# Kernel optimization log

Hardware: AMD Instinct MI355X
Metric: run time of the kernel (lower is better)

The kernel has to match this reference:

```python
import jax, jax.numpy as jnp
import numpy as np

N = 50000      # nodes
E = 800000     # edges (avg degree 16)
DIN = 128      # input_dim
DG = 128       # gnn_dim
DCLS = 128     # cls_dim
DOUT = 10      # output_dim
LMDA = 1.0     # rw_lmda
P_DROP = 0.5


def setup_inputs() -> dict:
    key = jax.random.key(0)
    ks = jax.random.split(key, 12)
    x = jax.random.normal(ks[0], (N, DIN), jnp.float32)
    edge_index = jax.random.randint(ks[1], (2, E), 0, N, dtype=jnp.int64)
    edge_weight = jax.random.uniform(ks[2], (E,), jnp.float32)
    def glorot(k, shape):
        lim = np.sqrt(6.0 / (shape[0] + shape[1])).astype(np.float32)
        return jax.random.uniform(k, shape, jnp.float32, -lim, lim)
    return dict(
        x=x, edge_index=edge_index, edge_weight=edge_weight,
        W_lin_in=glorot(ks[3], (DIN, DG)), b_lin_in=jnp.zeros((DG,), jnp.float32),
        W_agg_in=glorot(ks[4], (DG + DIN, DG)), b_agg_in=jnp.zeros((DG,), jnp.float32),
        W_lin_h=glorot(ks[5], (DG, DG)), b_lin_h=jnp.zeros((DG,), jnp.float32),
        W_agg_h=glorot(ks[6], (2 * DG, DG)), b_agg_h=jnp.zeros((DG,), jnp.float32),
        W_mlp1=glorot(ks[7], (DG, DCLS)), b_mlp1=jnp.zeros((DCLS,), jnp.float32),
        W_mlp2=glorot(ks[8], (DCLS, DOUT)), b_mlp2=jnp.zeros((DOUT,), jnp.float32),
    )


def _gs_layer(x, row, col, ew, inv_cnt, W_lin, b_lin, W_agg, b_agg):
    # GS_reweight: message = (1-lmda)*lin(x_j) + lmda*ew*lin(x_j), mean-aggregated
    # at row (flow='target_to_source': gather from col, scatter to row).
    h = x @ W_lin + b_lin                      # [N, DG] (lin before gather == lin(x_j))
    hj = h[col]                                # [E, DG] gather
    m = (1.0 - LMDA) * hj + LMDA * (ew[:, None] * hj)
    agg = jax.ops.segment_sum(m, row, num_segments=N) * inv_cnt[:, None]  # mean
    out = jnp.concatenate([agg, x], axis=-1) @ W_agg + b_agg              # update()
    return jax.nn.relu(out)


def _dropout(x, k):
    mask = jax.random.bernoulli(k, 1.0 - P_DROP, x.shape)
    return jnp.where(mask, x / (1.0 - P_DROP), 0.0)


def reference(x, edge_index, edge_weight,
              W_lin_in, b_lin_in, W_agg_in, b_agg_in,
              W_lin_h, b_lin_h, W_agg_h, b_agg_h,
              W_mlp1, b_mlp1, W_mlp2, b_mlp2):
    row, col = edge_index[0], edge_index[1]
    cnt = jax.ops.segment_sum(jnp.ones((E,), x.dtype), row, num_segments=N)
    inv_cnt = 1.0 / jnp.maximum(cnt, 1.0)     # scatter_mean: empty rows -> 0
    dk = jax.random.split(jax.random.key(42), 3)
    h = _gs_layer(x, row, col, edge_weight, inv_cnt, W_lin_in, b_lin_in, W_agg_in, b_agg_in)
    h = _dropout(jax.nn.relu(h), dk[0])       # relu is idempotent after update's relu
    for i in range(2):                        # layers 2,3 share prop_hidden weights
        h = _gs_layer(h, row, col, edge_weight, inv_cnt, W_lin_h, b_lin_h, W_agg_h, b_agg_h)
        h = _dropout(jax.nn.relu(h), dk[i + 1])
    y = jax.nn.relu(h @ W_mlp1 + b_mlp1) @ W_mlp2 + b_mlp2  # cls_layers=2, bn=False
    return (h, y)
```

## Files before the change

kernel.cpp:

```cpp
#include <hip/hip_runtime.h>
#include <cstdint>
#include <cstddef>


#define N_NODES 50000
#define N_EDGES 800000
#define DGN 128
#define DOUT 10
#define NELEM (N_NODES * DGN)
#define NMASKW (NELEM / 64)
#define NBINS 391
#define TILE 4096
#define NTILES ((N_EDGES + TILE - 1) / TILE)

#define XB_BLK 6250
#define MK_BLK 25000
#define HI_BLK NTILES
#define WC_BLK 128
#define TR_BLK 192
#define R0 XB_BLK
#define R1 (R0 + MK_BLK)
#define R2 (R1 + HI_BLK)
#define R3 (R2 + WC_BLK)
#define R4 (R3 + TR_BLK)
#define MEGA_BLOCKS (R4 + 1)

typedef __attribute__((ext_vector_type(8))) short bf16x8;
typedef __attribute__((ext_vector_type(4))) float f32x4;

__host__ __device__ static inline unsigned short f2bf(float f) {
  union { float f; unsigned u; } c; c.f = f;
  unsigned u = c.u;
  return (unsigned short)((u + 0x7fffu + ((u >> 16) & 1u)) >> 16);
}
__device__ static inline float bflo(unsigned u) { return __uint_as_float(u << 16); }
__device__ static inline float bfhi(unsigned u) { return __uint_as_float(u & 0xffff0000u); }

__host__ __device__ static inline void tf2x32(unsigned k0, unsigned k1,
                                              unsigned c0, unsigned c1,
                                              unsigned& o0, unsigned& o1) {
  unsigned ks2 = k0 ^ k1 ^ 0x1BD11BDAu;
  unsigned x0 = c0 + k0;
  unsigned x1 = c1 + k1;
#define TFR(r) { x0 += x1; x1 = (x1 << (r)) | (x1 >> (32 - (r))); x1 ^= x0; }
  TFR(13) TFR(15) TFR(26) TFR(6)
  x0 += k1;  x1 += ks2 + 1u;
  TFR(17) TFR(29) TFR(16) TFR(24)
  x0 += ks2; x1 += k0 + 2u;
  TFR(13) TFR(15) TFR(26) TFR(6)
  x0 += k0;  x1 += k1 + 3u;
  TFR(17) TFR(29) TFR(16) TFR(24)
  x0 += k1;  x1 += ks2 + 4u;
  TFR(13) TFR(15) TFR(26) TFR(6)
  x0 += ks2; x1 += k0 + 5u;
#undef TFR
  o0 = x0; o1 = x1;
}

__global__ __launch_bounds__(256) void mega_kernel(
    const float* __restrict__ x, unsigned short* __restrict__ xb,
    unsigned long long* __restrict__ m0, unsigned long long* __restrict__ m1,
    unsigned long long* __restrict__ m2,
    unsigned k00, unsigned k01, unsigned k10, unsigned k11,
    unsigned k20, unsigned k21,
    const int* __restrict__ ei, int* __restrict__ chist,
    const float* __restrict__ Wli, const float* __restrict__ Wai,
    const float* __restrict__ Wlh, const float* __restrict__ Wah,
    const float* __restrict__ Wm1,
    const float* __restrict__ bli, const float* __restrict__ blh,
    unsigned short* __restrict__ Tai, unsigned short* __restrict__ Tah,
    unsigned short* __restrict__ Tm1,
    float* __restrict__ bvi, float* __restrict__ bvh) {
  __shared__ int h[NBINS];
  const int b = blockIdx.x;
  const int tid = threadIdx.x;

  if (b < R0) {
    int g = b * 256 + tid;
    float4 v = ((const float4*)x)[g];
    ushort4 o;
    o.x = f2bf(v.x); o.y = f2bf(v.y); o.z = f2bf(v.z); o.w = f2bf(v.w);
    ((ushort4*)xb)[g] = o;
  } else if (b < R1) {
    int i = (b - R0) * 256 + tid;
    unsigned o0, o1;
    tf2x32(k00, k01, 0u, (unsigned)i, o0, o1);
    unsigned long long b0 = __ballot(((o0 ^ o1) >> 31) == 0u);
    tf2x32(k10, k11, 0u, (unsigned)i, o0, o1);
    unsigned long long b1 = __ballot(((o0 ^ o1) >> 31) == 0u);
    tf2x32(k20, k21, 0u, (unsigned)i, o0, o1);
    unsigned long long b2 = __ballot(((o0 ^ o1) >> 31) == 0u);
    if ((tid & 63) == 0) {
      int w = i >> 6;
      m0[w] = b0; m1[w] = b1; m2[w] = b2;
    }
  } else if (b < R2) {
    for (int i = tid; i < NBINS; i += 256) h[i] = 0;
    __syncthreads();
    const int e0 = (b - R1) * TILE;
#pragma unroll 4
    for (int j = 0; j < TILE; j += 256) {
      int e = e0 + j + tid;
      if (e < N_EDGES) {
        int r = ei[e];
        r = (r < 0) ? 0 : (r >= N_NODES ? N_NODES - 1 : r);
        atomicAdd(&h[r >> 7], 1);
      }
    }
    __syncthreads();
    for (int i = tid; i < NBINS; i += 256)
      if (h[i]) atomicAdd(&chist[i], h[i]);
  } else if (b < R3) {
    int idx = (b - R2) * 256 + tid;
    int n = idx & 127;
    int k = (idx >> 7) & 127;
    int m = idx >> 14;
    const float* Wl = m ? Wlh : Wli;
    const float* Wa = m ? Wah : Wai;
    unsigned short* T = m ? Tah : Tai;
    float acc = 0.0f;
#pragma unroll 8
    for (int j = 0; j < 128; ++j)
      acc += Wl[k * 128 + j] * Wa[j * 128 + n];
    T[n * 256 + k] = f2bf(acc);
  } else if (b < R4) {
    int j = (b - R3) * 256 + tid;
    if (j < 16384) {
      int kk = j & 127, n = j >> 7;
      Tai[n * 256 + 128 + kk] = f2bf(Wai[(size_t)(128 + kk) * 128 + n]);
    } else if (j < 32768) {
      int q = j - 16384;
      int kk = q & 127, n = q >> 7;
      Tah[n * 256 + 128 + kk] = f2bf(Wah[(size_t)(128 + kk) * 128 + n]);
    } else {
      int q = j - 32768;
      int k = q & 127, n = q >> 7;
      Tm1[n * 128 + k] = f2bf(Wm1[(size_t)k * 128 + n]);
    }
  } else {
    int n = tid & 127;
    const float* bl = (tid < 128) ? bli : blh;
    const float* Wa = (tid < 128) ? Wai : Wah;
    float acc = 0.0f;
    for (int j = 0; j < 128; ++j) acc += bl[j] * Wa[j * 128 + n];
    if (tid < 128) bvi[n] = acc; else bvh[n] = acc;
  }
}

__global__ __launch_bounds__(512) void prefix_kernel(const int* __restrict__ chist,
                                                     int* __restrict__ cbase,
                                                     int* __restrict__ ccursor,
                                                     int* __restrict__ rowptr) {
  __shared__ int s[512];
  const int t = threadIdx.x;
  int v = (t < NBINS) ? chist[t] : 0;
  s[t] = v;
  __syncthreads();
  for (int off = 1; off < 512; off <<= 1) {
    int tv = (t >= off) ? s[t - off] : 0;
    __syncthreads();
    s[t] += tv;
    __syncthreads();
  }
  if (t <= NBINS) {
    int ex = (t == 0) ? 0 : s[t - 1];
    cbase[t] = ex;
    if (t < NBINS) ccursor[t] = ex;
  }
  if (t == 0) rowptr[N_NODES] = N_EDGES;
}

__global__ __launch_bounds__(256) void scatter_kernel(const int* __restrict__ ei,
                                                      const float* __restrict__ ew,
                                                      int* __restrict__ ccursor,
                                                      uint2* __restrict__ pk) {
  __shared__ uint2 st[TILE];
  __shared__ unsigned short sbin[TILE];
  __shared__ int h[NBINS];
  __shared__ int base[NBINS];
  __shared__ int gbase[NBINS];
  __shared__ int cur[NBINS];
  __shared__ int sc[512];
  const int tid = threadIdx.x;
  const int e0 = blockIdx.x * TILE;
  const int nt = (N_EDGES - e0 < TILE) ? (N_EDGES - e0) : TILE;

  for (int i = tid; i < NBINS; i += 256) { h[i] = 0; cur[i] = 0; }
  __syncthreads();
  for (int j = tid; j < nt; j += 256) {
    int r = ei[e0 + j];
    r = (r < 0) ? 0 : (r >= N_NODES ? N_NODES - 1 : r);
    atomicAdd(&h[r >> 7], 1);
  }
  __syncthreads();
  sc[tid] = (tid < NBINS) ? h[tid] : 0;
  sc[tid + 256] = (tid + 256 < NBINS) ? h[tid + 256] : 0;
  __syncthreads();
  for (int off = 1; off < 512; off <<= 1) {
    int a0 = (tid >= off) ? sc[tid - off] : 0;
    int a1 = (tid + 256 >= off) ? sc[tid + 256 - off] : 0;
    __syncthreads();
    sc[tid] += a0; sc[tid + 256] += a1;
    __syncthreads();
  }
  if (tid < NBINS) {
    base[tid] = sc[tid] - h[tid];
    if (h[tid]) gbase[tid] = atomicAdd(&ccursor[tid], h[tid]);
  }
  if (tid + 256 < NBINS) {
    base[tid + 256] = sc[tid + 256] - h[tid + 256];
    if (h[tid + 256]) gbase[tid + 256] = atomicAdd(&ccursor[tid + 256], h[tid + 256]);
  }
  __syncthreads();
  for (int j = tid; j < nt; j += 256) {
    int r = ei[e0 + j];
    r = (r < 0) ? 0 : (r >= N_NODES ? N_NODES - 1 : r);
    int c = ei[N_EDGES + e0 + j];
    c = (c < 0) ? 0 : (c >= N_NODES ? N_NODES - 1 : c);
    int bb = r >> 7;
    int slot = base[bb] + atomicAdd(&cur[bb], 1);
    uint2 p;
    p.x = ((unsigned)r << 16) | (unsigned)c;
    p.y = __float_as_uint(ew[e0 + j]);
    st[slot] = p;
    sbin[slot] = (unsigned short)bb;
  }
  __syncthreads();
  for (int j = tid; j < nt; j += 256) {
    int bb = sbin[j];
    pk[gbase[bb] + (j - base[bb])] = st[j];
  }
}

__global__ __launch_bounds__(256) void place_kernel(const int* __restrict__ cbase,
                                                    const uint2* __restrict__ pk,
                                                    uint2* __restrict__ csr,
                                                    int* __restrict__ rowptr,
                                                    float* __restrict__ invc) {
  __shared__ int lcnt[128];
  __shared__ int lpre[128];
  __shared__ int lcur[128];
  __shared__ int sc[128];
  const int b = blockIdx.x;
  const int tid = threadIdx.x;
  const int cb = cbase[b];
  const int n = cbase[b + 1] - cb;
  const int r0 = b << 7;
  const int nr = (N_NODES - r0 < 128) ? (N_NODES - r0) : 128;

  if (tid < 128) { lcnt[tid] = 0; lcur[tid] = 0; }
  __syncthreads();
  for (int i = tid; i < n; i += 256) {
    int r7 = (int)(pk[cb + i].x >> 16) - r0;
    atomicAdd(&lcnt[r7], 1);
  }
  __syncthreads();
  if (tid < 128) sc[tid] = lcnt[tid];
  __syncthreads();
  for (int off = 1; off < 128; off <<= 1) {
    int tv = (tid >= off && tid < 128) ? sc[tid - off] : 0;
    __syncthreads();
    if (tid < 128) sc[tid] += tv;
    __syncthreads();
  }
  if (tid < 128) lpre[tid] = sc[tid] - lcnt[tid];
  __syncthreads();
  if (tid < nr) {
    rowptr[r0 + tid] = cb + lpre[tid];
    int c = lcnt[tid];
    invc[r0 + tid] = 1.0f / (float)(c > 1 ? c : 1);
  }
  for (int i = tid; i < n; i += 256) {
    uint2 p = pk[cb + i];
    int r7 = (int)(p.x >> 16) - r0;
    int slot = cb + lpre[r7] + atomicAdd(&lcur[r7], 1);
    uint2 o;
    o.x = p.x & 0xFFFFu;
    o.y = p.y;
    csr[slot] = o;
  }
}

__global__ __launch_bounds__(256) void agg_kernel(const unsigned short* __restrict__ hlin,
                                                  const int* __restrict__ rowptr,
                                                  const uint2* __restrict__ csr,
                                                  const float* __restrict__ invc,
                                                  unsigned short* __restrict__ agg,
                                                  float* __restrict__ swout) {
  const int r = blockIdx.x * 4 + (threadIdx.x >> 6);
  const int lane = threadIdx.x & 63;
  const int es = lane >> 4;
  const int cg = lane & 15;
  const int start = rowptr[r];
  const int num = rowptr[r + 1] - start;
  const uint4* __restrict__ H = (const uint4*)hlin;

  float a[8] = {0.f, 0.f, 0.f, 0.f, 0.f, 0.f, 0.f, 0.f};
  float ws = 0.f;
  for (int e = 0; e < num; e += 16) {
#pragma unroll
    for (int j = 0; j < 4; ++j) {
      int idx = e + j * 4 + es;
      bool ok = idx < num;
      int idxc = ok ? idx : (num - 1);
      uint2 q = csr[start + idxc];
      float w = ok ? __uint_as_float(q.y) : 0.0f;
      uint4 p = H[(size_t)q.x * 16 + cg];
      ws += w;
      a[0] += w * bflo(p.x); a[1] += w * bfhi(p.x);
      a[2] += w * bflo(p.y); a[3] += w * bfhi(p.y);
      a[4] += w * bflo(p.z); a[5] += w * bfhi(p.z);
      a[6] += w * bflo(p.w); a[7] += w * bfhi(p.w);
    }
  }
#pragma unroll
  for (int k = 0; k < 8; ++k) {
    a[k] += __shfl_xor(a[k], 32);
    a[k] += __shfl_xor(a[k], 16);
  }
  ws += __shfl_xor(ws, 32);
  ws += __shfl_xor(ws, 16);
  const float s = invc[r];
  if (es == 0) {
    uint4 o;
    o.x = (unsigned)f2bf(a[0] * s) | ((unsigned)f2bf(a[1] * s) << 16);
    o.y = (unsigned)f2bf(a[2] * s) | ((unsigned)f2bf(a[3] * s) << 16);
    o.z = (unsigned)f2bf(a[4] * s) | ((unsigned)f2bf(a[5] * s) << 16);
    o.w = (unsigned)f2bf(a[6] * s) | ((unsigned)f2bf(a[7] * s) << 16);
    ((uint4*)agg)[(size_t)r * 16 + cg] = o;
  }
  if (swout && lane == 0) swout[r] = ws * s;
}

template <int KTOT, bool RELU, bool MASK, bool SWB, bool WF32, bool WBF>
__global__ __launch_bounds__(256) void mfma_gemm(
    const unsigned short* __restrict__ A0, const unsigned short* __restrict__ A1,
    const unsigned short* __restrict__ Wt, const float* __restrict__ bias,
    const float* __restrict__ bias2, const float* __restrict__ sw,
    const unsigned long long* __restrict__ maskw,
    float* __restrict__ outf, unsigned short* __restrict__ outb) {
  constexpr int LDK = 72;
  __shared__ unsigned short Als[64 * LDK];
  __shared__ unsigned short Bls[64 * LDK];
  const int tid = threadIdx.x;
  const int mt = blockIdx.x >> 1;
  const int nt = blockIdx.x & 1;
  const int m0 = mt * 64;
  const int lane = tid & 63;
  const int wid = tid >> 6;
  const int wm = (wid >> 1) * 32;
  const int wn = (wid & 1) * 32;
  const int lrow = tid >> 2;
  const int lk = (tid & 3) * 16;

  int arow = m0 + lrow;
  if (arow >= N_NODES) arow = N_NODES - 1;

  f32x4 acc[2][2];
#pragma unroll
  for (int i = 0; i < 2; ++i)
#pragma unroll
    for (int j = 0; j < 2; ++j)
#pragma unroll
      for (int r = 0; r < 4; ++r) acc[i][j][r] = 0.0f;

  for (int kb = 0; kb < KTOT; kb += 64) {
    const unsigned short* Asrc = (kb < 128) ? A0 : A1;
    const unsigned short* ap = Asrc + (size_t)arow * 128 + (kb & 127) + lk;
    const unsigned short* bp = Wt + (size_t)(nt * 64 + lrow) * KTOT + kb + lk;
    unsigned short* al = &Als[lrow * LDK + lk];
    unsigned short* bl = &Bls[lrow * LDK + lk];
    *(uint4*)(al + 0) = *(const uint4*)(ap + 0);
    *(uint4*)(al + 8) = *(const uint4*)(ap + 8);
    *(uint4*)(bl + 0) = *(const uint4*)(bp + 0);
    *(uint4*)(bl + 8) = *(const uint4*)(bp + 8);
    __syncthreads();
#pragma unroll
    for (int ks = 0; ks < 64; ks += 32) {
      bf16x8 af[2], bfr[2];
#pragma unroll
      for (int t = 0; t < 2; ++t) {
        af[t]  = *(const bf16x8*)&Als[(wm + t * 16 + (lane & 15)) * LDK + ks + (lane >> 4) * 8];
        bfr[t] = *(const bf16x8*)&Bls[(wn + t * 16 + (lane & 15)) * LDK + ks + (lane >> 4) * 8];
      }
#pragma unroll
      for (int i = 0; i < 2; ++i)
#pragma unroll
        for (int j = 0; j < 2; ++j)
          acc[i][j] = __builtin_amdgcn_mfma_f32_16x16x32_bf16(af[i], bfr[j], acc[i][j], 0, 0, 0);
    }
    __syncthreads();
  }

  const int lm = lane >> 4;
  const int ln = lane & 15;
  float bcol[2], b2col[2];
#pragma unroll
  for (int j = 0; j < 2; ++j) {
    bcol[j] = bias[nt * 64 + wn + j * 16 + ln];
    b2col[j] = SWB ? bias2[nt * 64 + wn + j * 16 + ln] : 0.0f;
  }

#pragma unroll
  for (int i = 0; i < 2; ++i) {
    const int rbase = m0 + wm + i * 16 + lm * 4;
#pragma unroll
    for (int r = 0; r < 4; ++r) {
      const int row = rbase + r;
      if (row >= N_NODES) continue;
      unsigned long long mw = 0;
      if (MASK) mw = maskw[(size_t)row * 2 + nt];
      float swr = SWB ? sw[row] : 0.0f;
#pragma unroll
      for (int j = 0; j < 2; ++j) {
        const int col = nt * 64 + wn + j * 16 + ln;
        float v = acc[i][j][r] + (SWB ? (swr * bcol[j] + b2col[j]) : bcol[j]);
        if (RELU) v = fmaxf(v, 0.0f);
        if (MASK) v = ((mw >> (wn + j * 16 + ln)) & 1ull) ? 2.0f * v : 0.0f;
        if (WF32) outf[(size_t)row * DGN + col] = v;
        if (WBF)  outb[(size_t)row * DGN + col] = f2bf(v);
      }
    }
  }
}

__global__ __launch_bounds__(256) void mlp2_kernel(const unsigned short* __restrict__ t,
                                                   const float* __restrict__ W2,
                                                   const float* __restrict__ b2,
                                                   float* __restrict__ y) {
  __shared__ float Ws[128 * DOUT];
  __shared__ float bs[DOUT];
  for (int i = threadIdx.x; i < 128 * DOUT; i += 256) Ws[i] = W2[i];
  if (threadIdx.x < DOUT) bs[threadIdx.x] = b2[threadIdx.x];
  __syncthreads();
  int row = blockIdx.x * 256 + threadIdx.x;
  if (row >= N_NODES) return;
  float acc[DOUT];
#pragma unroll
  for (int c = 0; c < DOUT; ++c) acc[c] = bs[c];
  const uint4* tp = (const uint4*)(t + (size_t)row * 128);
#pragma unroll 4
  for (int k8 = 0; k8 < 16; ++k8) {
    uint4 raw = tp[k8];
    unsigned w[4] = {raw.x, raw.y, raw.z, raw.w};
#pragma unroll
    for (int p = 0; p < 4; ++p) {
      float lo = bflo(w[p]);
      float hi = bfhi(w[p]);
      const float* wr = &Ws[(k8 * 8 + p * 2) * DOUT];
#pragma unroll
      for (int c = 0; c < DOUT; ++c)
        acc[c] += lo * wr[c] + hi * wr[DOUT + c];
    }
  }
  float* yp = y + (size_t)row * DOUT;
#pragma unroll
  for (int c = 0; c < DOUT; ++c) yp[c] = acc[c];
}

extern "C" void kernel_launch(void* const* d_in, const int* in_sizes, int n_in,
                              void* d_out, int out_size, void* d_ws, size_t ws_size,
                              hipStream_t stream) {
  const float* x        = (const float*)d_in[0];
  const int*   ei       = (const int*)d_in[1];
  const float* ew       = (const float*)d_in[2];
  const float* W_lin_in = (const float*)d_in[3];
  const float* b_lin_in = (const float*)d_in[4];
  const float* W_agg_in = (const float*)d_in[5];
  const float* b_agg_in = (const float*)d_in[6];
  const float* W_lin_h  = (const float*)d_in[7];
  const float* b_lin_h  = (const float*)d_in[8];
  const float* W_agg_h  = (const float*)d_in[9];
  const float* b_agg_h  = (const float*)d_in[10];
  const float* W_mlp1   = (const float*)d_in[11];
  const float* b_mlp1   = (const float*)d_in[12];
  const float* W_mlp2   = (const float*)d_in[13];
  const float* b_mlp2   = (const float*)d_in[14];

  float* hout = (float*)d_out;
  float* yout = hout + (size_t)NELEM;

  char* p = (char*)d_ws;
  auto alloc = [&](size_t bytes) {
    char* q = p;
    p += (bytes + 255) & ~(size_t)255;
    return q;
  };
  int*   chist   = (int*)alloc((size_t)(NBINS + 1) * 4);
  int*   cbase   = (int*)alloc((size_t)(NBINS + 1) * 4);
  int*   ccursor = (int*)alloc((size_t)NBINS * 4);
  int*   rowptr  = (int*)alloc((size_t)(N_NODES + 1) * 4);
  float* invc    = (float*)alloc((size_t)N_NODES * 4);
  float* swv     = (float*)alloc((size_t)N_NODES * 4);
  uint2* pk      = (uint2*)alloc((size_t)N_EDGES * 8);
  uint2* csr     = (uint2*)alloc((size_t)N_EDGES * 8);
  unsigned short* xb   = (unsigned short*)alloc((size_t)NELEM * 2);
  unsigned short* aggb = (unsigned short*)alloc((size_t)NELEM * 2);
  unsigned short* hA   = (unsigned short*)alloc((size_t)NELEM * 2);
  unsigned short* hB   = (unsigned short*)alloc((size_t)NELEM * 2);
  unsigned long long* mw0 = (unsigned long long*)alloc((size_t)NMASKW * 8);
  unsigned long long* mw1 = (unsigned long long*)alloc((size_t)NMASKW * 8);
  unsigned long long* mw2 = (unsigned long long*)alloc((size_t)NMASKW * 8);
  unsigned short* Tai = (unsigned short*)alloc(32768 * 2);
  unsigned short* Tah = (unsigned short*)alloc(32768 * 2);
  unsigned short* Tm1 = (unsigned short*)alloc(16384 * 2);
  float* bvi = (float*)alloc(128 * 4);
  float* bvh = (float*)alloc(128 * 4);

  unsigned dk[3][2];
  for (unsigned i = 0; i < 3; ++i) tf2x32(0u, 42u, 0u, i, dk[i][0], dk[i][1]);

  const int NB = (N_NODES + 255) / 256;
  const int GB = ((N_NODES + 63) / 64) * 2;
  const int AB = (N_NODES + 3) / 4;

  hipMemsetAsync(chist, 0, (size_t)(NBINS + 1) * 4, stream);
  mega_kernel<<<MEGA_BLOCKS, 256, 0, stream>>>(
      x, xb, mw0, mw1, mw2,
      dk[0][0], dk[0][1], dk[1][0], dk[1][1], dk[2][0], dk[2][1],
      ei, chist, W_lin_in, W_agg_in, W_lin_h, W_agg_h, W_mlp1,
      b_lin_in, b_lin_h, Tai, Tah, Tm1, bvi, bvh);

  prefix_kernel<<<1, 512, 0, stream>>>(chist, cbase, ccursor, rowptr);
  scatter_kernel<<<NTILES, 256, 0, stream>>>(ei, ew, ccursor, pk);
  place_kernel<<<NBINS, 256, 0, stream>>>(cbase, pk, csr, rowptr, invc);

  agg_kernel<<<AB, 256, 0, stream>>>(xb, rowptr, csr, invc, aggb, swv);
  mfma_gemm<256, true, true, true, false, true><<<GB, 256, 0, stream>>>(
      aggb, xb, Tai, bvi, b_agg_in, swv, mw0, nullptr, hA);

  agg_kernel<<<AB, 256, 0, stream>>>(hA, rowptr, csr, invc, aggb, nullptr);
  mfma_gemm<256, true, true, true, false, true><<<GB, 256, 0, stream>>>(
      aggb, hA, Tah, bvh, b_agg_h, swv, mw1, nullptr, hB);

  agg_kernel<<<AB, 256, 0, stream>>>(hB, rowptr, csr, invc, aggb, nullptr);
  mfma_gemm<256, true, true, true, true, true><<<GB, 256, 0, stream>>>(
      aggb, hB, Tah, bvh, b_agg_h, swv, mw2, hout, hA);

  mfma_gemm<128, true, false, false, false, true><<<GB, 256, 0, stream>>>(
      hA, hA, Tm1, b_mlp1, nullptr, nullptr, mw0, nullptr, aggb);
  mlp2_kernel<<<NB, 256, 0, stream>>>(aggb, W_mlp2, b_mlp2, yout);
}
```

Measured before the change: 344.8 us.

## Move dropout mask generation into first aggregation and keep GEMM weights in registers

The Threefry dropout-mask blocks move out of the setup mega-kernel and are appended as extra blocks to the first aggregation launch. This lets the compute-heavy RNG run alongside the memory-bound gather instead of lengthening the setup stage. Separately, the MFMA GEMM now preloads each wave's weight fragments straight from global memory into registers once, dropping the B shared-memory tile and its per-step loads. This raises register pressure, since a K=256 GEMM holds 16 bf16x8 fragments, which could lower occupancy.

```diff
diff --git a/kernel.cpp b/kernel.cpp
--- a/kernel.cpp
+++ b/kernel.cpp
@@ -14,16 +14,17 @@
 #define NTILES ((N_EDGES + TILE - 1) / TILE)
 
 #define XB_BLK 6250
-#define MK_BLK 25000
 #define HI_BLK NTILES
 #define WC_BLK 128
 #define TR_BLK 192
 #define R0 XB_BLK
-#define R1 (R0 + MK_BLK)
-#define R2 (R1 + HI_BLK)
-#define R3 (R2 + WC_BLK)
-#define R4 (R3 + TR_BLK)
-#define MEGA_BLOCKS (R4 + 1)
+#define R1 (R0 + HI_BLK)
+#define R2 (R1 + WC_BLK)
+#define R3 (R2 + TR_BLK)
+#define MEGA_BLOCKS (R3 + 1)
+
+#define AB_BLOCKS ((N_NODES + 3) / 4)
+#define MK_BLOCKS 25000
 
 typedef __attribute__((ext_vector_type(8))) short bf16x8;
 typedef __attribute__((ext_vector_type(4))) float f32x4;
@@ -59,10 +60,6 @@
 
 __global__ __launch_bounds__(256) void mega_kernel(
     const float* __restrict__ x, unsigned short* __restrict__ xb,
-    unsigned long long* __restrict__ m0, unsigned long long* __restrict__ m1,
-    unsigned long long* __restrict__ m2,
-    unsigned k00, unsigned k01, unsigned k10, unsigned k11,
-    unsigned k20, unsigned k21,
     const int* __restrict__ ei, int* __restrict__ chist,
     const float* __restrict__ Wli, const float* __restrict__ Wai,
     const float* __restrict__ Wlh, const float* __restrict__ Wah,
@@ -82,22 +79,9 @@
     o.x = f2bf(v.x); o.y = f2bf(v.y); o.z = f2bf(v.z); o.w = f2bf(v.w);
     ((ushort4*)xb)[g] = o;
   } else if (b < R1) {
-    int i = (b - R0) * 256 + tid;
-    unsigned o0, o1;
-    tf2x32(k00, k01, 0u, (unsigned)i, o0, o1);
-    unsigned long long b0 = __ballot(((o0 ^ o1) >> 31) == 0u);
-    tf2x32(k10, k11, 0u, (unsigned)i, o0, o1);
-    unsigned long long b1 = __ballot(((o0 ^ o1) >> 31) == 0u);
-    tf2x32(k20, k21, 0u, (unsigned)i, o0, o1);
-    unsigned long long b2 = __ballot(((o0 ^ o1) >> 31) == 0u);
-    if ((tid & 63) == 0) {
-      int w = i >> 6;
-      m0[w] = b0; m1[w] = b1; m2[w] = b2;
-    }
-  } else if (b < R2) {
     for (int i = tid; i < NBINS; i += 256) h[i] = 0;
     __syncthreads();
-    const int e0 = (b - R1) * TILE;
+    const int e0 = (b - R0) * TILE;
 #pragma unroll 4
     for (int j = 0; j < TILE; j += 256) {
       int e = e0 + j + tid;
@@ -110,8 +94,8 @@
     __syncthreads();
     for (int i = tid; i < NBINS; i += 256)
       if (h[i]) atomicAdd(&chist[i], h[i]);
-  } else if (b < R3) {
-    int idx = (b - R2) * 256 + tid;
+  } else if (b < R2) {
+    int idx = (b - R1) * 256 + tid;
     int n = idx & 127;
     int k = (idx >> 7) & 127;
     int m = idx >> 14;
@@ -123,8 +107,8 @@
     for (int j = 0; j < 128; ++j)
       acc += Wl[k * 128 + j] * Wa[j * 128 + n];
     T[n * 256 + k] = f2bf(acc);
-  } else if (b < R4) {
-    int j = (b - R3) * 256 + tid;
+  } else if (b < R3) {
+    int j = (b - R2) * 256 + tid;
     if (j < 16384) {
       int kk = j & 127, n = j >> 7;
       Tai[n * 256 + 128 + kk] = f2bf(Wai[(size_t)(128 + kk) * 128 + n]);
@@ -286,7 +270,28 @@
                                                   const uint2* __restrict__ csr,
                                                   const float* __restrict__ invc,
                                                   unsigned short* __restrict__ agg,
-                                                  float* __restrict__ swout) {
+                                                  float* __restrict__ swout,
+                                                  unsigned long long* __restrict__ m0,
+                                                  unsigned long long* __restrict__ m1,
+                                                  unsigned long long* __restrict__ m2,
+                                                  unsigned k00, unsigned k01,
+                                                  unsigned k10, unsigned k11,
+                                                  unsigned k20, unsigned k21) {
+  if (blockIdx.x >= AB_BLOCKS) {
+    int i = (blockIdx.x - AB_BLOCKS) * 256 + threadIdx.x;
+    unsigned o0, o1;
+    tf2x32(k00, k01, 0u, (unsigned)i, o0, o1);
+    unsigned long long b0 = __ballot(((o0 ^ o1) >> 31) == 0u);
+    tf2x32(k10, k11, 0u, (unsigned)i, o0, o1);
+    unsigned long long b1 = __ballot(((o0 ^ o1) >> 31) == 0u);
+    tf2x32(k20, k21, 0u, (unsigned)i, o0, o1);
+    unsigned long long b2 = __ballot(((o0 ^ o1) >> 31) == 0u);
+    if ((threadIdx.x & 63) == 0) {
+      int w = i >> 6;
+      m0[w] = b0; m1[w] = b1; m2[w] = b2;
+    }
+    return;
+  }
   const int r = blockIdx.x * 4 + (threadIdx.x >> 6);
   const int lane = threadIdx.x & 63;
   const int es = lane >> 4;
@@ -340,8 +345,8 @@
     const unsigned long long* __restrict__ maskw,
     float* __restrict__ outf, unsigned short* __restrict__ outb) {
   constexpr int LDK = 72;
+  constexpr int NKF = KTOT / 32;
   __shared__ unsigned short Als[64 * LDK];
-  __shared__ unsigned short Bls[64 * LDK];
   const int tid = threadIdx.x;
   const int mt = blockIdx.x >> 1;
   const int nt = blockIdx.x & 1;
@@ -352,9 +357,19 @@
   const int wn = (wid & 1) * 32;
   const int lrow = tid >> 2;
   const int lk = (tid & 3) * 16;
+  const int ln = lane & 15;
+  const int lh = lane >> 4;
 
   int arow = m0 + lrow;
   if (arow >= N_NODES) arow = N_NODES - 1;
+
+  bf16x8 bfr[NKF][2];
+#pragma unroll
+  for (int kf = 0; kf < NKF; ++kf)
+#pragma unroll
+    for (int j = 0; j < 2; ++j)
+      bfr[kf][j] = *(const bf16x8*)(Wt +
+          (size_t)(nt * 64 + wn + j * 16 + ln) * KTOT + kf * 32 + lh * 8);
 
   f32x4 acc[2][2];
 #pragma unroll
@@ -367,33 +382,27 @@
   for (int kb = 0; kb < KTOT; kb += 64) {
     const unsigned short* Asrc = (kb < 128) ? A0 : A1;
     const unsigned short* ap = Asrc + (size_t)arow * 128 + (kb & 127) + lk;
-    const unsigned short* bp = Wt + (size_t)(nt * 64 + lrow) * KTOT + kb + lk;
     unsigned short* al = &Als[lrow * LDK + lk];
-    unsigned short* bl = &Bls[lrow * LDK + lk];
     *(uint4*)(al + 0) = *(const uint4*)(ap + 0);
     *(uint4*)(al + 8) = *(const uint4*)(ap + 8);
-    *(uint4*)(bl + 0) = *(const uint4*)(bp + 0);
-    *(uint4*)(bl + 8) = *(const uint4*)(bp + 8);
     __syncthreads();
 #pragma unroll
     for (int ks = 0; ks < 64; ks += 32) {
-      bf16x8 af[2], bfr[2];
-#pragma unroll
-      for (int t = 0; t < 2; ++t) {
-        af[t]  = *(const bf16x8*)&Als[(wm + t * 16 + (lane & 15)) * LDK + ks + (lane >> 4) * 8];
-        bfr[t] = *(const bf16x8*)&Bls[(wn + t * 16 + (lane & 15)) * LDK + ks + (lane >> 4) * 8];
-      }
+      const int kf = (kb + ks) >> 5;
+      bf16x8 af[2];
+#pragma unroll
+      for (int t = 0; t < 2; ++t)
+        af[t] = *(const bf16x8*)&Als[(wm + t * 16 + ln) * LDK + ks + lh * 8];
 #pragma unroll
       for (int i = 0; i < 2; ++i)
 #pragma unroll
         for (int j = 0; j < 2; ++j)
-          acc[i][j] = __builtin_amdgcn_mfma_f32_16x16x32_bf16(af[i], bfr[j], acc[i][j], 0, 0, 0);
+          acc[i][j] = __builtin_amdgcn_mfma_f32_16x16x32_bf16(af[i], bfr[kf][j], acc[i][j], 0, 0, 0);
     }
     __syncthreads();
   }
 
   const int lm = lane >> 4;
-  const int ln = lane & 15;
   float bcol[2], b2col[2];
 #pragma unroll
   for (int j = 0; j < 2; ++j) {
@@ -512,28 +521,29 @@
 
   const int NB = (N_NODES + 255) / 256;
   const int GB = ((N_NODES + 63) / 64) * 2;
-  const int AB = (N_NODES + 3) / 4;
 
   hipMemsetAsync(chist, 0, (size_t)(NBINS + 1) * 4, stream);
   mega_kernel<<<MEGA_BLOCKS, 256, 0, stream>>>(
-      x, xb, mw0, mw1, mw2,
-      dk[0][0], dk[0][1], dk[1][0], dk[1][1], dk[2][0], dk[2][1],
-      ei, chist, W_lin_in, W_agg_in, W_lin_h, W_agg_h, W_mlp1,
+      x, xb, ei, chist, W_lin_in, W_agg_in, W_lin_h, W_agg_h, W_mlp1,
       b_lin_in, b_lin_h, Tai, Tah, Tm1, bvi, bvh);
 
   prefix_kernel<<<1, 512, 0, stream>>>(chist, cbase, ccursor, rowptr);
   scatter_kernel<<<NTILES, 256, 0, stream>>>(ei, ew, ccursor, pk);
   place_kernel<<<NBINS, 256, 0, stream>>>(cbase, pk, csr, rowptr, invc);
 
-  agg_kernel<<<AB, 256, 0, stream>>>(xb, rowptr, csr, invc, aggb, swv);
+  agg_kernel<<<AB_BLOCKS + MK_BLOCKS, 256, 0, stream>>>(
+      xb, rowptr, csr, invc, aggb, swv, mw0, mw1, mw2,
+      dk[0][0], dk[0][1], dk[1][0], dk[1][1], dk[2][0], dk[2][1]);
   mfma_gemm<256, true, true, true, false, true><<<GB, 256, 0, stream>>>(
       aggb, xb, Tai, bvi, b_agg_in, swv, mw0, nullptr, hA);
 
-  agg_kernel<<<AB, 256, 0, stream>>>(hA, rowptr, csr, invc, aggb, nullptr);
+  agg_kernel<<<AB_BLOCKS, 256, 0, stream>>>(
+      hA, rowptr, csr, invc, aggb, nullptr, mw0, mw1, mw2, 0, 0, 0, 0, 0, 0);
   mfma_gemm<256, true, true, true, false, true><<<GB, 256, 0, stream>>>(
       aggb, hA, Tah, bvh, b_agg_h, swv, mw1, nullptr, hB);
 
-  agg_kernel<<<AB, 256, 0, stream>>>(hB, rowptr, csr, invc, aggb, nullptr);
+  agg_kernel<<<AB_BLOCKS, 256, 0, stream>>>(
+      hB, rowptr, csr, invc, aggb, nullptr, mw0, mw1, mw2, 0, 0, 0, 0, 0, 0);
   mfma_gemm<256, true, true, true, true, true><<<GB, 256, 0, stream>>>(
       aggb, hB, Tah, bvh, b_agg_h, swv, mw2, hout, hA);
 
```

Result: slower. 376.6 us (+9.2%).

## Fuse neighbor aggregation into per-layer GEMM and spread dropout mask generation

Applied to the files above, without the earlier changes.

Each GNN layer now runs as one kernel. A block of 64 rows gathers and mean-aggregates neighbor features into shared memory, then runs the MFMA GEMM over the aggregated and self features for the full 128 output columns. This removes the bf16 aggregate buffer round-trip and the separate edge-weight-sum array. Dropout mask generation moves out of the mega kernel: the first mask is built by extra blocks in the scatter kernel, the other two by extra blocks in the first fused layer. In exchange, each block serializes the gather phase before its GEMM, and only about 782 blocks do layer work.

```diff
diff --git a/kernel.cpp b/kernel.cpp
--- a/kernel.cpp
+++ b/kernel.cpp
@@ -12,18 +12,18 @@
 #define NBINS 391
 #define TILE 4096
 #define NTILES ((N_EDGES + TILE - 1) / TILE)
+#define GBF ((N_NODES + 63) / 64)
+#define MK_BLOCKS 25000
 
 #define XB_BLK 6250
-#define MK_BLK 25000
 #define HI_BLK NTILES
 #define WC_BLK 128
 #define TR_BLK 192
 #define R0 XB_BLK
-#define R1 (R0 + MK_BLK)
-#define R2 (R1 + HI_BLK)
-#define R3 (R2 + WC_BLK)
-#define R4 (R3 + TR_BLK)
-#define MEGA_BLOCKS (R4 + 1)
+#define R1 (R0 + HI_BLK)
+#define R2 (R1 + WC_BLK)
+#define R3 (R2 + TR_BLK)
+#define MEGA_BLOCKS (R3 + 1)
 
 typedef __attribute__((ext_vector_type(8))) short bf16x8;
 typedef __attribute__((ext_vector_type(4))) float f32x4;
@@ -59,10 +59,6 @@
 
 __global__ __launch_bounds__(256) void mega_kernel(
     const float* __restrict__ x, unsigned short* __restrict__ xb,
-    unsigned long long* __restrict__ m0, unsigned long long* __restrict__ m1,
-    unsigned long long* __restrict__ m2,
-    unsigned k00, unsigned k01, unsigned k10, unsigned k11,
-    unsigned k20, unsigned k21,
     const int* __restrict__ ei, int* __restrict__ chist,
     const float* __restrict__ Wli, const float* __restrict__ Wai,
     const float* __restrict__ Wlh, const float* __restrict__ Wah,
@@ -82,22 +78,9 @@
     o.x = f2bf(v.x); o.y = f2bf(v.y); o.z = f2bf(v.z); o.w = f2bf(v.w);
     ((ushort4*)xb)[g] = o;
   } else if (b < R1) {
-    int i = (b - R0) * 256 + tid;
-    unsigned o0, o1;
-    tf2x32(k00, k01, 0u, (unsigned)i, o0, o1);
-    unsigned long long b0 = __ballot(((o0 ^ o1) >> 31) == 0u);
-    tf2x32(k10, k11, 0u, (unsigned)i, o0, o1);
-    unsigned long long b1 = __ballot(((o0 ^ o1) >> 31) == 0u);
-    tf2x32(k20, k21, 0u, (unsigned)i, o0, o1);
-    unsigned long long b2 = __ballot(((o0 ^ o1) >> 31) == 0u);
-    if ((tid & 63) == 0) {
-      int w = i >> 6;
-      m0[w] = b0; m1[w] = b1; m2[w] = b2;
-    }
-  } else if (b < R2) {
     for (int i = tid; i < NBINS; i += 256) h[i] = 0;
     __syncthreads();
-    const int e0 = (b - R1) * TILE;
+    const int e0 = (b - R0) * TILE;
 #pragma unroll 4
     for (int j = 0; j < TILE; j += 256) {
       int e = e0 + j + tid;
@@ -110,8 +93,8 @@
     __syncthreads();
     for (int i = tid; i < NBINS; i += 256)
       if (h[i]) atomicAdd(&chist[i], h[i]);
-  } else if (b < R3) {
-    int idx = (b - R2) * 256 + tid;
+  } else if (b < R2) {
+    int idx = (b - R1) * 256 + tid;
     int n = idx & 127;
     int k = (idx >> 7) & 127;
     int m = idx >> 14;
@@ -123,8 +106,8 @@
     for (int j = 0; j < 128; ++j)
       acc += Wl[k * 128 + j] * Wa[j * 128 + n];
     T[n * 256 + k] = f2bf(acc);
-  } else if (b < R4) {
-    int j = (b - R3) * 256 + tid;
+  } else if (b < R3) {
+    int j = (b - R2) * 256 + tid;
     if (j < 16384) {
       int kk = j & 127, n = j >> 7;
       Tai[n * 256 + 128 + kk] = f2bf(Wai[(size_t)(128 + kk) * 128 + n]);
@@ -173,7 +156,17 @@
 __global__ __launch_bounds__(256) void scatter_kernel(const int* __restrict__ ei,
                                                       const float* __restrict__ ew,
                                                       int* __restrict__ ccursor,
-                                                      uint2* __restrict__ pk) {
+                                                      uint2* __restrict__ pk,
+                                                      unsigned long long* __restrict__ mg0,
+                                                      unsigned k00, unsigned k01) {
+  if (blockIdx.x >= NTILES) {
+    int i = (blockIdx.x - NTILES) * 256 + threadIdx.x;
+    unsigned o0, o1;
+    tf2x32(k00, k01, 0u, (unsigned)i, o0, o1);
+    unsigned long long b0 = __ballot(((o0 ^ o1) >> 31) == 0u);
+    if ((threadIdx.x & 63) == 0) mg0[i >> 6] = b0;
+    return;
+  }
   __shared__ uint2 st[TILE];
   __shared__ unsigned short sbin[TILE];
   __shared__ int h[NBINS];
@@ -281,64 +274,177 @@
   }
 }
 
-__global__ __launch_bounds__(256) void agg_kernel(const unsigned short* __restrict__ hlin,
-                                                  const int* __restrict__ rowptr,
-                                                  const uint2* __restrict__ csr,
-                                                  const float* __restrict__ invc,
-                                                  unsigned short* __restrict__ agg,
-                                                  float* __restrict__ swout) {
-  const int r = blockIdx.x * 4 + (threadIdx.x >> 6);
-  const int lane = threadIdx.x & 63;
-  const int es = lane >> 4;
-  const int cg = lane & 15;
-  const int start = rowptr[r];
-  const int num = rowptr[r + 1] - start;
-  const uint4* __restrict__ H = (const uint4*)hlin;
-
-  float a[8] = {0.f, 0.f, 0.f, 0.f, 0.f, 0.f, 0.f, 0.f};
-  float ws = 0.f;
-  for (int e = 0; e < num; e += 16) {
-#pragma unroll
-    for (int j = 0; j < 4; ++j) {
-      int idx = e + j * 4 + es;
-      bool ok = idx < num;
-      int idxc = ok ? idx : (num - 1);
-      uint2 q = csr[start + idxc];
-      float w = ok ? __uint_as_float(q.y) : 0.0f;
-      uint4 p = H[(size_t)q.x * 16 + cg];
-      ws += w;
-      a[0] += w * bflo(p.x); a[1] += w * bfhi(p.x);
-      a[2] += w * bflo(p.y); a[3] += w * bfhi(p.y);
-      a[4] += w * bflo(p.z); a[5] += w * bfhi(p.z);
-      a[6] += w * bflo(p.w); a[7] += w * bfhi(p.w);
-    }
-  }
-#pragma unroll
-  for (int k = 0; k < 8; ++k) {
-    a[k] += __shfl_xor(a[k], 32);
-    a[k] += __shfl_xor(a[k], 16);
-  }
-  ws += __shfl_xor(ws, 32);
-  ws += __shfl_xor(ws, 16);
-  const float s = invc[r];
-  if (es == 0) {
-    uint4 o;
-    o.x = (unsigned)f2bf(a[0] * s) | ((unsigned)f2bf(a[1] * s) << 16);
-    o.y = (unsigned)f2bf(a[2] * s) | ((unsigned)f2bf(a[3] * s) << 16);
-    o.z = (unsigned)f2bf(a[4] * s) | ((unsigned)f2bf(a[5] * s) << 16);
-    o.w = (unsigned)f2bf(a[6] * s) | ((unsigned)f2bf(a[7] * s) << 16);
-    ((uint4*)agg)[(size_t)r * 16 + cg] = o;
-  }
-  if (swout && lane == 0) swout[r] = ws * s;
-}
-
-template <int KTOT, bool RELU, bool MASK, bool SWB, bool WF32, bool WBF>
+template <bool L3, bool MASKGEN>
+__global__ __launch_bounds__(256) void fused_layer(
+    const unsigned short* __restrict__ Hin,
+    const int* __restrict__ rowptr, const uint2* __restrict__ csr,
+    const float* __restrict__ invc,
+    const unsigned short* __restrict__ Wt,
+    const float* __restrict__ bvec, const float* __restrict__ bagg,
+    const unsigned long long* __restrict__ maskw,
+    float* __restrict__ outf, unsigned short* __restrict__ outb,
+    unsigned long long* __restrict__ g1, unsigned long long* __restrict__ g2,
+    unsigned k10, unsigned k11, unsigned k20, unsigned k21) {
+  if (MASKGEN && blockIdx.x >= GBF) {
+    int i = (blockIdx.x - GBF) * 256 + threadIdx.x;
+    unsigned o0, o1;
+    tf2x32(k10, k11, 0u, (unsigned)i, o0, o1);
+    unsigned long long b1 = __ballot(((o0 ^ o1) >> 31) == 0u);
+    tf2x32(k20, k21, 0u, (unsigned)i, o0, o1);
+    unsigned long long b2 = __ballot(((o0 ^ o1) >> 31) == 0u);
+    if ((threadIdx.x & 63) == 0) { g1[i >> 6] = b1; g2[i >> 6] = b2; }
+    return;
+  }
+  constexpr int LA = 136;
+  constexpr int LS = 72;
+  __shared__ unsigned short aggT[64 * LA];
+  __shared__ unsigned short Als[64 * LS];
+  __shared__ unsigned short Bls[128 * LS];
+  __shared__ float swL[64];
+  const int tid = threadIdx.x;
+  const int m0 = blockIdx.x * 64;
+  const int lane = tid & 63;
+  const int wid = tid >> 6;
+
+  {
+    const int es = lane >> 4;
+    const int cg = lane & 15;
+    const uint4* __restrict__ H4 = (const uint4*)Hin;
+    for (int rr = wid; rr < 64; rr += 4) {
+      int r = m0 + rr;
+      if (r >= N_NODES) r = N_NODES - 1;
+      const int start = rowptr[r];
+      const int num = rowptr[r + 1] - start;
+      float a[8] = {0.f, 0.f, 0.f, 0.f, 0.f, 0.f, 0.f, 0.f};
+      float ws = 0.f;
+      for (int e = 0; e < num; e += 16) {
+#pragma unroll
+        for (int j = 0; j < 4; ++j) {
+          int idx = e + j * 4 + es;
+          bool ok = idx < num;
+          int idxc = ok ? idx : (num - 1);
+          uint2 q = csr[start + idxc];
+          float w = ok ? __uint_as_float(q.y) : 0.0f;
+          uint4 p = H4[(size_t)q.x * 16 + cg];
+          ws += w;
+          a[0] += w * bflo(p.x); a[1] += w * bfhi(p.x);
+          a[2] += w * bflo(p.y); a[3] += w * bfhi(p.y);
+          a[4] += w * bflo(p.z); a[5] += w * bfhi(p.z);
+          a[6] += w * bflo(p.w); a[7] += w * bfhi(p.w);
+        }
+      }
+#pragma unroll
+      for (int k = 0; k < 8; ++k) {
+        a[k] += __shfl_xor(a[k], 32);
+        a[k] += __shfl_xor(a[k], 16);
+      }
+      ws += __shfl_xor(ws, 32);
+      ws += __shfl_xor(ws, 16);
+      const float s = invc[r];
+      if (es == 0) {
+        uint4 o;
+        o.x = (unsigned)f2bf(a[0] * s) | ((unsigned)f2bf(a[1] * s) << 16);
+        o.y = (unsigned)f2bf(a[2] * s) | ((unsigned)f2bf(a[3] * s) << 16);
+        o.z = (unsigned)f2bf(a[4] * s) | ((unsigned)f2bf(a[5] * s) << 16);
+        o.w = (unsigned)f2bf(a[6] * s) | ((unsigned)f2bf(a[7] * s) << 16);
+        *(uint4*)&aggT[rr * LA + cg * 8] = o;
+      }
+      if (lane == 0) swL[rr] = ws * s;
+    }
+  }
+  __syncthreads();
+
+  const int wm = (wid >> 1) * 32;
+  const int wn = (wid & 1) * 64;
+  const int ln = lane & 15;
+  const int lh = lane >> 4;
+  const int sArow = tid >> 2;
+  const int sAk = (tid & 3) * 16;
+  const int sBcol = tid >> 1;
+  const int sBk = (tid & 1) * 32;
+  int arow = m0 + sArow;
+  if (arow >= N_NODES) arow = N_NODES - 1;
+
+  f32x4 acc[2][4];
+#pragma unroll
+  for (int i = 0; i < 2; ++i)
+#pragma unroll
+    for (int j = 0; j < 4; ++j)
+#pragma unroll
+      for (int r = 0; r < 4; ++r) acc[i][j][r] = 0.0f;
+
+  for (int kb = 0; kb < 256; kb += 64) {
+    if (kb >= 128) {
+      const unsigned short* ap = Hin + (size_t)arow * 128 + (kb & 127) + sAk;
+      unsigned short* al = &Als[sArow * LS + sAk];
+      *(uint4*)(al + 0) = *(const uint4*)(ap + 0);
+      *(uint4*)(al + 8) = *(const uint4*)(ap + 8);
+    }
+    {
+      const unsigned short* bp = Wt + (size_t)sBcol * 256 + kb + sBk;
+      unsigned short* bl = &Bls[sBcol * LS + sBk];
+      *(uint4*)(bl + 0)  = *(const uint4*)(bp + 0);
+      *(uint4*)(bl + 8)  = *(const uint4*)(bp + 8);
+      *(uint4*)(bl + 16) = *(const uint4*)(bp + 16);
+      *(uint4*)(bl + 24) = *(const uint4*)(bp + 24);
+    }
+    __syncthreads();
+#pragma unroll
+    for (int ks = 0; ks < 64; ks += 32) {
+      bf16x8 af[2], bfr[4];
+#pragma unroll
+      for (int i = 0; i < 2; ++i)
+        af[i] = (kb < 128)
+          ? *(const bf16x8*)&aggT[(wm + i * 16 + ln) * LA + kb + ks + lh * 8]
+          : *(const bf16x8*)&Als[(wm + i * 16 + ln) * LS + ks + lh * 8];
+#pragma unroll
+      for (int j = 0; j < 4; ++j)
+        bfr[j] = *(const bf16x8*)&Bls[(wn + j * 16 + ln) * LS + ks + lh * 8];
+#pragma unroll
+      for (int i = 0; i < 2; ++i)
+#pragma unroll
+        for (int j = 0; j < 4; ++j)
+          acc[i][j] = __builtin_amdgcn_mfma_f32_16x16x32_bf16(af[i], bfr[j], acc[i][j], 0, 0, 0);
+    }
+    __syncthreads();
+  }
+
+  const int lm = lane >> 4;
+  float bc[4], b2[4];
+#pragma unroll
+  for (int j = 0; j < 4; ++j) {
+    int col = wn + j * 16 + ln;
+    bc[j] = bvec[col];
+    b2[j] = bagg[col];
+  }
+#pragma unroll
+  for (int i = 0; i < 2; ++i) {
+    const int lr0 = wm + i * 16 + lm * 4;
+#pragma unroll
+    for (int r = 0; r < 4; ++r) {
+      const int lr = lr0 + r;
+      const int row = m0 + lr;
+      if (row >= N_NODES) continue;
+      const float swr = swL[lr];
+      const unsigned long long mw = maskw[(size_t)row * 2 + (wn >> 6)];
+#pragma unroll
+      for (int j = 0; j < 4; ++j) {
+        const int col = wn + j * 16 + ln;
+        float v = acc[i][j][r] + swr * bc[j] + b2[j];
+        v = fmaxf(v, 0.0f);
+        v = ((mw >> (col & 63)) & 1ull) ? 2.0f * v : 0.0f;
+        if (L3) outf[(size_t)row * DGN + col] = v;
+        outb[(size_t)row * DGN + col] = f2bf(v);
+      }
+    }
+  }
+}
+
+template <int KTOT, bool RELU>
 __global__ __launch_bounds__(256) void mfma_gemm(
-    const unsigned short* __restrict__ A0, const unsigned short* __restrict__ A1,
+    const unsigned short* __restrict__ A0,
     const unsigned short* __restrict__ Wt, const float* __restrict__ bias,
-    const float* __restrict__ bias2, const float* __restrict__ sw,
-    const unsigned long long* __restrict__ maskw,
-    float* __restrict__ outf, unsigned short* __restrict__ outb) {
+    unsigned short* __restrict__ outb) {
   constexpr int LDK = 72;
   __shared__ unsigned short Als[64 * LDK];
   __shared__ unsigned short Bls[64 * LDK];
@@ -365,8 +471,7 @@
       for (int r = 0; r < 4; ++r) acc[i][j][r] = 0.0f;
 
   for (int kb = 0; kb < KTOT; kb += 64) {
-    const unsigned short* Asrc = (kb < 128) ? A0 : A1;
-    const unsigned short* ap = Asrc + (size_t)arow * 128 + (kb & 127) + lk;
+    const unsigned short* ap = A0 + (size_t)arow * 128 + (kb & 127) + lk;
     const unsigned short* bp = Wt + (size_t)(nt * 64 + lrow) * KTOT + kb + lk;
     unsigned short* al = &Als[lrow * LDK + lk];
     unsigned short* bl = &Bls[lrow * LDK + lk];
@@ -394,12 +499,9 @@
 
   const int lm = lane >> 4;
   const int ln = lane & 15;
-  float bcol[2], b2col[2];
-#pragma unroll
-  for (int j = 0; j < 2; ++j) {
-    bcol[j] = bias[nt * 64 + wn + j * 16 + ln];
-    b2col[j] = SWB ? bias2[nt * 64 + wn + j * 16 + ln] : 0.0f;
-  }
+  float bcol[2];
+#pragma unroll
+  for (int j = 0; j < 2; ++j) bcol[j] = bias[nt * 64 + wn + j * 16 + ln];
 
 #pragma unroll
   for (int i = 0; i < 2; ++i) {
@@ -408,17 +510,12 @@
     for (int r = 0; r < 4; ++r) {
       const int row = rbase + r;
       if (row >= N_NODES) continue;
-      unsigned long long mw = 0;
-      if (MASK) mw = maskw[(size_t)row * 2 + nt];
-      float swr = SWB ? sw[row] : 0.0f;
 #pragma unroll
       for (int j = 0; j < 2; ++j) {
         const int col = nt * 64 + wn + j * 16 + ln;
-        float v = acc[i][j][r] + (SWB ? (swr * bcol[j] + b2col[j]) : bcol[j]);
+        float v = acc[i][j][r] + bcol[j];
         if (RELU) v = fmaxf(v, 0.0f);
-        if (MASK) v = ((mw >> (wn + j * 16 + ln)) & 1ull) ? 2.0f * v : 0.0f;
-        if (WF32) outf[(size_t)row * DGN + col] = v;
-        if (WBF)  outb[(size_t)row * DGN + col] = f2bf(v);
+        outb[(size_t)row * DGN + col] = f2bf(v);
       }
     }
   }
@@ -491,11 +588,10 @@
   int*   ccursor = (int*)alloc((size_t)NBINS * 4);
   int*   rowptr  = (int*)alloc((size_t)(N_NODES + 1) * 4);
   float* invc    = (float*)alloc((size_t)N_NODES * 4);
-  float* swv     = (float*)alloc((size_t)N_NODES * 4);
   uint2* pk      = (uint2*)alloc((size_t)N_EDGES * 8);
   uint2* csr     = (uint2*)alloc((size_t)N_EDGES * 8);
   unsigned short* xb   = (unsigned short*)alloc((size_t)NELEM * 2);
-  unsigned short* aggb = (unsigned short*)alloc((size_t)NELEM * 2);
+  unsigned short* tmb  = (unsigned short*)alloc((size_t)NELEM * 2);
   unsigned short* hA   = (unsigned short*)alloc((size_t)NELEM * 2);
   unsigned short* hB   = (unsigned short*)alloc((size_t)NELEM * 2);
   unsigned long long* mw0 = (unsigned long long*)alloc((size_t)NMASKW * 8);
@@ -512,32 +608,29 @@
 
   const int NB = (N_NODES + 255) / 256;
   const int GB = ((N_NODES + 63) / 64) * 2;
-  const int AB = (N_NODES + 3) / 4;
 
   hipMemsetAsync(chist, 0, (size_t)(NBINS + 1) * 4, stream);
   mega_kernel<<<MEGA_BLOCKS, 256, 0, stream>>>(
-      x, xb, mw0, mw1, mw2,
-      dk[0][0], dk[0][1], dk[1][0], dk[1][1], dk[2][0], dk[2][1],
-      ei, chist, W_lin_in, W_agg_in, W_lin_h, W_agg_h, W_mlp1,
+      x, xb, ei, chist, W_lin_in, W_agg_in, W_lin_h, W_agg_h, W_mlp1,
       b_lin_in, b_lin_h, Tai, Tah, Tm1, bvi, bvh);
 
   prefix_kernel<<<1, 512, 0, stream>>>(chist, cbase, ccursor, rowptr);
-  scatter_kernel<<<NTILES, 256, 0, stream>>>(ei, ew, ccursor, pk);
+  scatter_kernel<<<NTILES + MK_BLOCKS, 256, 0, stream>>>(
+      ei, ew, ccursor, pk, mw0, dk[0][0], dk[0][1]);
   place_kernel<<<NBINS, 256, 0, stream>>>(cbase, pk, csr, rowptr, invc);
 
-  agg_kernel<<<AB, 256, 0, stream>>>(xb, rowptr, csr, invc, aggb, swv);
-  mfma_gemm<256, true, true, true, false, true><<<GB, 256, 0, stream>>>(
-      aggb, xb, Tai, bvi, b_agg_in, swv, mw0, nullptr, hA);
-
-  agg_kernel<<<AB, 256, 0, stream>>>(hA, rowptr, csr, invc, aggb, nullptr);
-  mfma_gemm<256, true, true, true, false, true><<<GB, 256, 0, stream>>>(
-      aggb, hA, Tah, bvh, b_agg_h, swv, mw1, nullptr, hB);
-
-  agg_kernel<<<AB, 256, 0, stream>>>(hB, rowptr, csr, invc, aggb, nullptr);
-  mfma_gemm<256, true, true, true, true, true><<<GB, 256, 0, stream>>>(
-      aggb, hB, Tah, bvh, b_agg_h, swv, mw2, hout, hA);
-
-  mfma_gemm<128, true, false, false, false, true><<<GB, 256, 0, stream>>>(
-      hA, hA, Tm1, b_mlp1, nullptr, nullptr, mw0, nullptr, aggb);
-  mlp2_kernel<<<NB, 256, 0, stream>>>(aggb, W_mlp2, b_mlp2, yout);
-}
+  fused_layer<false, true><<<GBF + MK_BLOCKS, 256, 0, stream>>>(
+      xb, rowptr, csr, invc, Tai, bvi, b_agg_in, mw0, nullptr, hA,
+      mw1, mw2, dk[1][0], dk[1][1], dk[2][0], dk[2][1]);
+
+  fused_layer<false, false><<<GBF, 256, 0, stream>>>(
+      hA, rowptr, csr, invc, Tah, bvh, b_agg_h, mw1, nullptr, hB,
+      nullptr, nullptr, 0, 0, 0, 0);
+
+  fused_layer<true, false><<<GBF, 256, 0, stream>>>(
+      hB, rowptr, csr, invc, Tah, bvh, b_agg_h, mw2, hout, hA,
+      nullptr, nullptr, 0, 0, 0, 0);
+
+  mfma_gemm<128, true><<<GB, 256, 0, stream>>>(hA, Tm1, b_mlp1, tmb);
+  mlp2_kernel<<<NB, 256, 0, stream>>>(tmb, W_mlp2, b_mlp2, yout);
+}
```

New measurement: 493.3 us. 43.1% more time.
